# Kernel tuning notes

Hardware: AMD Instinct MI355X
Metric: run time of the kernel (lower is better)

Reference implementation:

```python
import jax, jax.numpy as jnp
import numpy as np

B, H, W = 64, 16, 16
DIMS = [2048, 1024, 512, 256, 128, 1]


def _target_fc(x, w, b):
    # x: [B, in, H, W]; w: [B, out, in, 1, 1]; b: [B, out]
    # Equivalent to grouped 1x1 conv2d with groups=B (per-sample FC over channels).
    y = jnp.einsum('boi,bihw->bohw', w[:, :, :, 0, 0], x)
    return y + b[:, :, None, None]


def setup_inputs() -> dict:
    key = jax.random.key(0)
    ks = jax.random.split(key, 11)
    inp = {'x': jax.random.normal(ks[0], (B, DIMS[0], H, W), dtype=jnp.float32)}
    for i in range(5):
        din, dout = DIMS[i], DIMS[i + 1]
        scale = 1.0 / np.sqrt(din)
        inp[f'w{i+1}'] = jax.random.normal(ks[1 + 2 * i], (B, dout, din, 1, 1), dtype=jnp.float32) * scale
        inp[f'b{i+1}'] = jax.random.normal(ks[2 + 2 * i], (B, dout), dtype=jnp.float32) * scale
    return inp


def reference(x, w1, b1, w2, b2, w3, b3, w4, b4, w5, b5):
    q = jax.nn.sigmoid(_target_fc(x, w1, b1))
    q = jax.nn.sigmoid(_target_fc(q, w2, b2))
    q = jax.nn.sigmoid(_target_fc(q, w3, b3))
    q = jax.nn.sigmoid(_target_fc(q, w4, b4))
    q = _target_fc(q, w5, b5)
    return jnp.squeeze(q)  # [B, H, W]
```

## Files before the change

kernel.cpp:

```cpp
#include <hip/hip_runtime.h>
#include <hip/hip_bf16.h>
#include <cstdint>

#define DEVINL __device__ __forceinline__

typedef __attribute__((ext_vector_type(8))) short bf16x8;
typedef __attribute__((ext_vector_type(4))) float f32x4;

DEVINL unsigned short f2bf(float f) {
    union { float f; unsigned u; } v; v.f = f;
    unsigned r = v.u + 0x7fffu + ((v.u >> 16) & 1u);
    return (unsigned short)(r >> 16);
}
DEVINL float bf2f(unsigned short h) {
    union { unsigned u; float f; } v; v.u = ((unsigned)h) << 16;
    return v.f;
}

constexpr int BM = 64, BN = 256, BK = 32;
constexpr int NSP   = 256;
constexpr int SABUF = 64 * 32;
constexpr int SBUF  = 256 * 32;

__global__ __launch_bounds__(256)
void xpose(const float* __restrict__ x, unsigned short* __restrict__ xT)
{
    __shared__ float sh[64][65];
    const int b   = blockIdx.y;
    const int kt  = blockIdx.x & 31;
    const int ntb = blockIdx.x >> 5;
    const int k0 = kt * 64, n0 = ntb * 64;

    const int r = threadIdx.x >> 4;
    const int c = (threadIdx.x & 15) * 4;

    const float* xb = x + ((size_t)b * 2048 + k0) * 256 + n0;
#pragma unroll
    for (int i = 0; i < 4; ++i) {
        float4 v = *(const float4*)(xb + (size_t)(r + 16 * i) * 256 + c);
        sh[r + 16 * i][c + 0] = v.x;
        sh[r + 16 * i][c + 1] = v.y;
        sh[r + 16 * i][c + 2] = v.z;
        sh[r + 16 * i][c + 3] = v.w;
    }
    __syncthreads();
#pragma unroll
    for (int i = 0; i < 4; ++i) {
        const int rr = r + 16 * i;
        ushort4 o;
        o.x = f2bf(sh[c + 0][rr]);
        o.y = f2bf(sh[c + 1][rr]);
        o.z = f2bf(sh[c + 2][rr]);
        o.w = f2bf(sh[c + 3][rr]);
        *(ushort4*)(xT + ((size_t)b * NSP + n0 + rr) * 2048 + k0 + c) = o;
    }
}

__global__ __launch_bounds__(256, 4)
void fc_gemm(const float* __restrict__ Wt, const float* __restrict__ bias,
             const unsigned short* __restrict__ X, unsigned short* __restrict__ Yt,
             int M, int K)
{
    const int b  = blockIdx.x;
    const int m0 = blockIdx.y * BM;

    __shared__ __align__(128) unsigned short pool[2 * SABUF + 2 * SBUF];
    unsigned short* sA = pool;
    unsigned short* sB = pool + 2 * SABUF;

    const int tid  = threadIdx.x;
    const int lane = tid & 63;
    const int wid  = tid >> 6;
    const int wn   = wid * 64;
    const int fr   = lane & 15;
    const int fo   = (lane >> 4) * 8;

    const int am = tid >> 2, ac = (tid & 3) * 8;
    const float* Wb = Wt + (size_t)b * M * K + (size_t)m0 * K + (size_t)am * K + ac;

    const int grow = wid * 64 + (lane >> 2);
    const int gchk = ((lane & 3) ^ ((lane >> 3) & 3)) * 8;
    const unsigned short* Xb = X + (size_t)b * NSP * K;

    const int bslot = ((lane >> 4) ^ ((fr >> 1) & 3)) * 8;

    const int NT = K / BK;

    float4 aS[2];

#define LOADA(k0) { aS[0] = *(const float4*)(Wb + (k0)); \
                    aS[1] = *(const float4*)(Wb + (k0) + 4); }
#define STOREA(p) { uint4 w_; \
        w_.x = (unsigned)f2bf(aS[0].x) | ((unsigned)f2bf(aS[0].y) << 16); \
        w_.y = (unsigned)f2bf(aS[0].z) | ((unsigned)f2bf(aS[0].w) << 16); \
        w_.z = (unsigned)f2bf(aS[1].x) | ((unsigned)f2bf(aS[1].y) << 16); \
        w_.w = (unsigned)f2bf(aS[1].z) | ((unsigned)f2bf(aS[1].w) << 16); \
        *(uint4*)&sA[(p) * SABUF + am * 32 + ac] = w_; }
#define GLOADB(k0, p) { \
    _Pragma("unroll") for (int i = 0; i < 4; ++i) { \
        const unsigned short* src_ = Xb + (size_t)(grow + i * 16) * K + (k0) + gchk; \
        const unsigned short* dst_ = sB + (p) * SBUF + (wid * 64 + i * 16) * 32; \
        __builtin_amdgcn_global_load_lds( \
            (const __attribute__((address_space(1))) void*)src_, \
            (__attribute__((address_space(3))) void*)dst_, 16, 0, 0); } }

    f32x4 acc[4][4] = {};

    GLOADB(0, 0)
    LOADA(0)
    STOREA(0)
    __syncthreads();

#pragma unroll 1
    for (int t = 0; t < NT; ++t) {
        const int p = t & 1;
        if (t + 1 < NT) { LOADA((t + 1) * BK) GLOADB((t + 1) * BK, p ^ 1) }

        bf16x8 af[4], bfv[4];
#pragma unroll
        for (int i = 0; i < 4; ++i)
            af[i] = *(const bf16x8*)&sA[p * SABUF + (i * 16 + fr) * 32 + fo];
#pragma unroll
        for (int i = 0; i < 4; ++i)
            bfv[i] = *(const bf16x8*)&sB[p * SBUF + (wn + i * 16 + fr) * 32 + bslot];

#pragma unroll
        for (int mi = 0; mi < 4; ++mi)
#pragma unroll
            for (int ni = 0; ni < 4; ++ni)
                acc[mi][ni] = __builtin_amdgcn_mfma_f32_16x16x32_bf16(af[mi], bfv[ni], acc[mi][ni], 0, 0, 0);

        if (t + 1 < NT) STOREA(p ^ 1)

        __syncthreads();
    }
#undef LOADA
#undef STOREA
#undef GLOADB

    const int hi4 = (lane >> 4) * 4;
#pragma unroll 1
    for (int ph = 0; ph < 2; ++ph) {
        if ((wn >> 7) == ph) {
#pragma unroll
            for (int mi = 0; mi < 4; ++mi) {
#pragma unroll
                for (int ni = 0; ni < 4; ++ni) {
                    const int r  = (wn & 127) + ni * 16 + fr;
                    const int mb = mi * 16 + hi4;
                    f32x4 v = acc[mi][ni];
                    ushort4 o;
#pragma unroll
                    for (int q = 0; q < 4; ++q) {
                        float yv = v[q] + bias[(size_t)b * M + m0 + mb + q];
                        yv = 1.0f / (1.0f + __expf(-yv));
                        ((unsigned short*)&o)[q] = f2bf(yv);
                    }
                    *(ushort4*)&pool[r * 72 + mb] = o;
                }
            }
        }
        __syncthreads();
        const int r = tid >> 3;
        const int c = (tid & 7) * 8;
#pragma unroll
        for (int it = 0; it < 4; ++it) {
            const int rr = r + it * 32;
            uint4 v = *(const uint4*)&pool[rr * 72 + c];
            *(uint4*)&Yt[((size_t)b * NSP + ph * 128 + rr) * M + m0 + c] = v;
        }
        __syncthreads();
    }
}

__global__ void fc_final(const unsigned short* __restrict__ A4,
                         const float* __restrict__ W5,
                         const float* __restrict__ B5,
                         float* __restrict__ out)
{
    const int b = blockIdx.x;
    const int t = threadIdx.x;
    const unsigned short* row = A4 + ((size_t)b * NSP + t) * 128;
    const float* w = W5 + (size_t)b * 128;
    float acc = B5[b];
#pragma unroll
    for (int k = 0; k < 128; k += 8) {
        uint4 v = *(const uint4*)(row + k);
        acc += bf2f((unsigned short)(v.x & 0xffff)) * w[k+0];
        acc += bf2f((unsigned short)(v.x >> 16))    * w[k+1];
        acc += bf2f((unsigned short)(v.y & 0xffff)) * w[k+2];
        acc += bf2f((unsigned short)(v.y >> 16))    * w[k+3];
        acc += bf2f((unsigned short)(v.z & 0xffff)) * w[k+4];
        acc += bf2f((unsigned short)(v.z >> 16))    * w[k+5];
        acc += bf2f((unsigned short)(v.w & 0xffff)) * w[k+6];
        acc += bf2f((unsigned short)(v.w >> 16))    * w[k+7];
    }
    out[b * NSP + t] = acc;
}

extern "C" void kernel_launch(void* const* d_in, const int* in_sizes, int n_in,
                              void* d_out, int out_size, void* d_ws, size_t ws_size,
                              hipStream_t stream)
{
    const float* x  = (const float*)d_in[0];
    const float* w1 = (const float*)d_in[1];
    const float* b1 = (const float*)d_in[2];
    const float* w2 = (const float*)d_in[3];
    const float* b2 = (const float*)d_in[4];
    const float* w3 = (const float*)d_in[5];
    const float* b3 = (const float*)d_in[6];
    const float* w4 = (const float*)d_in[7];
    const float* b4 = (const float*)d_in[8];
    const float* w5 = (const float*)d_in[9];
    const float* b5 = (const float*)d_in[10];

    unsigned short* ws0 = (unsigned short*)d_ws;

    const size_t XT = (size_t)64 * 256 * 2048;
    unsigned short* xT   = ws0;
    unsigned short* act1 = ws0 + XT;
    unsigned short* act2 = ws0;
    unsigned short* act3 = ws0 + (size_t)64 * 256 * 512;
    unsigned short* act4 = ws0 + (size_t)64 * 256 * (512 + 256);

    xpose<<<dim3(128, 64), dim3(256), 0, stream>>>(x, xT);
    fc_gemm<<<dim3(64, 16), dim3(256), 0, stream>>>(w1, b1, xT,   act1, 1024, 2048);
    fc_gemm<<<dim3(64,  8), dim3(256), 0, stream>>>(w2, b2, act1, act2,  512, 1024);
    fc_gemm<<<dim3(64,  4), dim3(256), 0, stream>>>(w3, b3, act2, act3,  256,  512);
    fc_gemm<<<dim3(64,  2), dim3(256), 0, stream>>>(w4, b4, act3, act4,  128,  256);
    fc_final<<<dim3(64), dim3(256), 0, stream>>>(act4, w5, b5, (float*)d_out);
}
```

Before: 357.7 us.

## Make GEMM waves independent: per-wave LDS slices, register A fragments, barrier-free pipeline

Each wave now streams its own 64-column slice of X into a private double-buffered LDS region. The fp32 weight rows are loaded straight into registers in MFMA fragment layout and converted there, so the A tile no longer goes through shared memory. All __syncthreads are removed in favour of per-wave s_waitcnt control, and the epilogue writes activations directly to global memory instead of staging through LDS. BM is halved to 32, doubling the grid, which trades more weight-row and X re-reads and uncoalesced 8-byte output stores for fewer barriers and more parallelism.

```diff
diff --git a/kernel.cpp b/kernel.cpp
--- a/kernel.cpp
+++ b/kernel.cpp
@@ -17,10 +17,18 @@
     return v.f;
 }
 
-constexpr int BM = 64, BN = 256, BK = 32;
-constexpr int NSP   = 256;
-constexpr int SABUF = 64 * 32;
-constexpr int SBUF  = 256 * 32;
+DEVINL bf16x8 cvt8(float4 lo, float4 hi) {
+    bf16x8 r;
+    r[0] = (short)f2bf(lo.x); r[1] = (short)f2bf(lo.y);
+    r[2] = (short)f2bf(lo.z); r[3] = (short)f2bf(lo.w);
+    r[4] = (short)f2bf(hi.x); r[5] = (short)f2bf(hi.y);
+    r[6] = (short)f2bf(hi.z); r[7] = (short)f2bf(hi.w);
+    return r;
+}
+
+constexpr int BM = 32, BN = 256, BK = 32;
+constexpr int NSP = 256;
+constexpr int SLICE = 64 * 32;
 
 __global__ __launch_bounds__(256)
 void xpose(const float* __restrict__ x, unsigned short* __restrict__ xT)
@@ -64,112 +72,95 @@
     const int b  = blockIdx.x;
     const int m0 = blockIdx.y * BM;
 
-    __shared__ __align__(128) unsigned short pool[2 * SABUF + 2 * SBUF];
-    unsigned short* sA = pool;
-    unsigned short* sB = pool + 2 * SABUF;
+    __shared__ __align__(128) unsigned short sB[4 * 2 * SLICE];
 
     const int tid  = threadIdx.x;
     const int lane = tid & 63;
     const int wid  = tid >> 6;
     const int wn   = wid * 64;
     const int fr   = lane & 15;
-    const int fo   = (lane >> 4) * 8;
-
-    const int am = tid >> 2, ac = (tid & 3) * 8;
-    const float* Wb = Wt + (size_t)b * M * K + (size_t)m0 * K + (size_t)am * K + ac;
-
-    const int grow = wid * 64 + (lane >> 2);
-    const int gchk = ((lane & 3) ^ ((lane >> 3) & 3)) * 8;
-    const unsigned short* Xb = X + (size_t)b * NSP * K;
-
+    const int fo8  = (lane >> 4) * 8;
+
+    unsigned short* mySB = sB + wid * (2 * SLICE);
+
+    const float* wr0 = Wt + (size_t)b * M * K + (size_t)(m0 + fr) * K + fo8;
+    const float* wr1 = wr0 + (size_t)16 * K;
+
+    const int grow  = lane >> 2;
+    const int gchk  = ((lane & 3) ^ ((lane >> 3) & 3)) * 8;
     const int bslot = ((lane >> 4) ^ ((fr >> 1) & 3)) * 8;
+    const unsigned short* Xb = X + ((size_t)b * NSP + wn) * K;
 
     const int NT = K / BK;
 
-    float4 aS[2];
-
-#define LOADA(k0) { aS[0] = *(const float4*)(Wb + (k0)); \
-                    aS[1] = *(const float4*)(Wb + (k0) + 4); }
-#define STOREA(p) { uint4 w_; \
-        w_.x = (unsigned)f2bf(aS[0].x) | ((unsigned)f2bf(aS[0].y) << 16); \
-        w_.y = (unsigned)f2bf(aS[0].z) | ((unsigned)f2bf(aS[0].w) << 16); \
-        w_.z = (unsigned)f2bf(aS[1].x) | ((unsigned)f2bf(aS[1].y) << 16); \
-        w_.w = (unsigned)f2bf(aS[1].z) | ((unsigned)f2bf(aS[1].w) << 16); \
-        *(uint4*)&sA[(p) * SABUF + am * 32 + ac] = w_; }
+    float4 aA[4], aB[4];
+
+#define LOADA(SET, k0) { \
+        SET[0] = *(const float4*)(wr0 + (k0));     \
+        SET[1] = *(const float4*)(wr0 + (k0) + 4); \
+        SET[2] = *(const float4*)(wr1 + (k0));     \
+        SET[3] = *(const float4*)(wr1 + (k0) + 4); }
 #define GLOADB(k0, p) { \
     _Pragma("unroll") for (int i = 0; i < 4; ++i) { \
         const unsigned short* src_ = Xb + (size_t)(grow + i * 16) * K + (k0) + gchk; \
-        const unsigned short* dst_ = sB + (p) * SBUF + (wid * 64 + i * 16) * 32; \
+        unsigned short* dst_ = mySB + (p) * SLICE + (i * 16) * 32; \
         __builtin_amdgcn_global_load_lds( \
             (const __attribute__((address_space(1))) void*)src_, \
             (__attribute__((address_space(3))) void*)dst_, 16, 0, 0); } }
 
-    f32x4 acc[4][4] = {};
+    f32x4 acc[2][4] = {};
 
     GLOADB(0, 0)
-    LOADA(0)
-    STOREA(0)
-    __syncthreads();
+    LOADA(aA, 0)
+    GLOADB(BK, 1)
+    LOADA(aB, BK)
+    asm volatile("s_waitcnt vmcnt(8)" ::: "memory");
+
+#define KSTEP(t_, SET) { \
+    const int tt = (t_); const int p = tt & 1; \
+    bf16x8 af0 = cvt8(SET[0], SET[1]); \
+    bf16x8 af1 = cvt8(SET[2], SET[3]); \
+    bf16x8 bfv[4]; \
+    _Pragma("unroll") for (int i = 0; i < 4; ++i) \
+        bfv[i] = *(const bf16x8*)&mySB[p * SLICE + (i * 16 + fr) * 32 + bslot]; \
+    _Pragma("unroll") for (int ni = 0; ni < 4; ++ni) { \
+        acc[0][ni] = __builtin_amdgcn_mfma_f32_16x16x32_bf16(af0, bfv[ni], acc[0][ni], 0, 0, 0); \
+        acc[1][ni] = __builtin_amdgcn_mfma_f32_16x16x32_bf16(af1, bfv[ni], acc[1][ni], 0, 0, 0); } \
+    asm volatile("s_waitcnt lgkmcnt(0)" ::: "memory");   \
+    if (tt + 2 < NT) { \
+        GLOADB((tt + 2) * BK, p)       \
+        LOADA(SET, (tt + 2) * BK)      \
+        asm volatile("s_waitcnt vmcnt(8)" ::: "memory");   \
+    } else { \
+        asm volatile("s_waitcnt vmcnt(0)" ::: "memory");   \
+    } }
 
 #pragma unroll 1
-    for (int t = 0; t < NT; ++t) {
-        const int p = t & 1;
-        if (t + 1 < NT) { LOADA((t + 1) * BK) GLOADB((t + 1) * BK, p ^ 1) }
-
-        bf16x8 af[4], bfv[4];
-#pragma unroll
-        for (int i = 0; i < 4; ++i)
-            af[i] = *(const bf16x8*)&sA[p * SABUF + (i * 16 + fr) * 32 + fo];
-#pragma unroll
-        for (int i = 0; i < 4; ++i)
-            bfv[i] = *(const bf16x8*)&sB[p * SBUF + (wn + i * 16 + fr) * 32 + bslot];
-
-#pragma unroll
-        for (int mi = 0; mi < 4; ++mi)
-#pragma unroll
-            for (int ni = 0; ni < 4; ++ni)
-                acc[mi][ni] = __builtin_amdgcn_mfma_f32_16x16x32_bf16(af[mi], bfv[ni], acc[mi][ni], 0, 0, 0);
-
-        if (t + 1 < NT) STOREA(p ^ 1)
-
-        __syncthreads();
-    }
+    for (int t = 0; t < NT; t += 2) {
+        KSTEP(t,     aA)
+        KSTEP(t + 1, aB)
+    }
+#undef KSTEP
 #undef LOADA
-#undef STOREA
 #undef GLOADB
 
     const int hi4 = (lane >> 4) * 4;
-#pragma unroll 1
-    for (int ph = 0; ph < 2; ++ph) {
-        if ((wn >> 7) == ph) {
-#pragma unroll
-            for (int mi = 0; mi < 4; ++mi) {
-#pragma unroll
-                for (int ni = 0; ni < 4; ++ni) {
-                    const int r  = (wn & 127) + ni * 16 + fr;
-                    const int mb = mi * 16 + hi4;
-                    f32x4 v = acc[mi][ni];
-                    ushort4 o;
-#pragma unroll
-                    for (int q = 0; q < 4; ++q) {
-                        float yv = v[q] + bias[(size_t)b * M + m0 + mb + q];
-                        yv = 1.0f / (1.0f + __expf(-yv));
-                        ((unsigned short*)&o)[q] = f2bf(yv);
-                    }
-                    *(ushort4*)&pool[r * 72 + mb] = o;
-                }
+#pragma unroll
+    for (int mi = 0; mi < 2; ++mi) {
+#pragma unroll
+        for (int ni = 0; ni < 4; ++ni) {
+            const int n  = wn + ni * 16 + fr;
+            const int mb = m0 + mi * 16 + hi4;
+            f32x4 v = acc[mi][ni];
+            ushort4 o;
+#pragma unroll
+            for (int q = 0; q < 4; ++q) {
+                float yv = v[q] + bias[(size_t)b * M + mb + q];
+                yv = 1.0f / (1.0f + __expf(-yv));
+                ((unsigned short*)&o)[q] = f2bf(yv);
             }
+            *(ushort4*)&Yt[((size_t)b * NSP + n) * M + mb] = o;
         }
-        __syncthreads();
-        const int r = tid >> 3;
-        const int c = (tid & 7) * 8;
-#pragma unroll
-        for (int it = 0; it < 4; ++it) {
-            const int rr = r + it * 32;
-            uint4 v = *(const uint4*)&pool[rr * 72 + c];
-            *(uint4*)&Yt[((size_t)b * NSP + ph * 128 + rr) * M + m0 + c] = v;
-        }
-        __syncthreads();
     }
 }
 
@@ -224,9 +215,9 @@
     unsigned short* act4 = ws0 + (size_t)64 * 256 * (512 + 256);
 
     xpose<<<dim3(128, 64), dim3(256), 0, stream>>>(x, xT);
-    fc_gemm<<<dim3(64, 16), dim3(256), 0, stream>>>(w1, b1, xT,   act1, 1024, 2048);
-    fc_gemm<<<dim3(64,  8), dim3(256), 0, stream>>>(w2, b2, act1, act2,  512, 1024);
-    fc_gemm<<<dim3(64,  4), dim3(256), 0, stream>>>(w3, b3, act2, act3,  256,  512);
-    fc_gemm<<<dim3(64,  2), dim3(256), 0, stream>>>(w4, b4, act3, act4,  128,  256);
+    fc_gemm<<<dim3(64, 32), dim3(256), 0, stream>>>(w1, b1, xT,   act1, 1024, 2048);
+    fc_gemm<<<dim3(64, 16), dim3(256), 0, stream>>>(w2, b2, act1, act2,  512, 1024);
+    fc_gemm<<<dim3(64,  8), dim3(256), 0, stream>>>(w3, b3, act2, act3,  256,  512);
+    fc_gemm<<<dim3(64,  4), dim3(256), 0, stream>>>(w4, b4, act3, act4,  128,  256);
     fc_final<<<dim3(64), dim3(256), 0, stream>>>(act4, w5, b5, (float*)d_out);
 }
```

After: 598.0 us. +67.2%, slower.
